# Kernel tuning notes

Measured on AMD Instinct MI355X. Metric: run time of the kernel, lower is better.

## Reference

```python
import jax, jax.numpy as jnp
import numpy as np

NUM_MEL = 80
STACK_FRAMES = 4   # encoder.embed.right_context + 1
STRIDE = 4         # encoder.embed.subsampling_rate
N_SUB = 1          # n_subsequent
NCB = 1            # num_codebooks
EMB_DIM = 16
NUM_EMB = 8192
ENC_DIM = 512
B, T = 16, 2048
T_ENC = (T - STACK_FRAMES) // STRIDE + 1  # 512
EPS_LN = 1e-6


def setup_inputs() -> dict:
    key = jax.random.key(0)
    k = jax.random.split(key, 6)
    feats = jax.random.normal(k[0], (B, T, NUM_MEL), dtype=jnp.float32)
    feats_lengths = jax.random.randint(k[1], (B,), T // 2, T + 1, dtype=jnp.int32)
    encoder_out = jax.random.normal(k[2], (B, T_ENC, ENC_DIM), dtype=jnp.float32)
    in_dim = NUM_MEL * STRIDE
    lim = float(np.sqrt(6.0 / (in_dim + EMB_DIM * NCB)))  # xavier-uniform
    projection = jax.random.uniform(k[3], (in_dim, EMB_DIM * NCB), jnp.float32, -lim, lim)
    emb = jax.random.normal(k[4], (NUM_EMB, NCB, EMB_DIM), dtype=jnp.float32)
    embeddings = emb / (jnp.linalg.norm(emb, axis=-1, keepdims=True) + 1e-8)
    top_n_out = 0.02 * jax.random.normal(k[5], (N_SUB, NCB, ENC_DIM, NUM_EMB), dtype=jnp.float32)
    return {"feats": feats, "feats_lengths": feats_lengths, "encoder_out": encoder_out,
            "projection": projection, "embeddings": embeddings, "top_n_out": top_n_out}


def _stack_features(feats, lens):
    b, t, f = feats.shape
    n = (t - STACK_FRAMES) // STRIDE + 1
    idx = jnp.arange(n)[:, None] * STRIDE + jnp.arange(STACK_FRAMES)[None, :]  # [n, S]
    stack = feats[:, idx, :].reshape(b, n, STACK_FRAMES * f)                   # [B, n, S*F]
    mask = jnp.arange(t)[None, :] < lens[:, None]                              # [B, T]
    sub_mask = jnp.all(mask[:, idx], axis=-1)                                  # [B, n]
    mean = stack.mean(-1, keepdims=True)
    var = stack.var(-1, keepdims=True)
    stack = (stack - mean) * jax.lax.rsqrt(var + EPS_LN)  # LayerNorm, no affine
    return stack, sub_mask


def _nearest_idx(stack, projection, embeddings):
    x = stack @ projection                                         # [B, n, ncb*E]
    x = x / (jnp.linalg.norm(x, axis=-1, keepdims=True) + 1e-8)
    b, n, _ = x.shape
    v, ncb, e = embeddings.shape
    xf = x.reshape(b * n, ncb, e)
    dots = jnp.einsum('nce,vce->ncv', xf, embeddings)              # [N, ncb, V]
    x2 = jnp.sum(xf * xf, -1, keepdims=True)                       # [N, ncb, 1]
    e2 = jnp.sum(embeddings * embeddings, -1).T[None]              # [1, ncb, V]
    dist = x2 - 2.0 * dots + e2
    codes = jnp.argmin(dist, axis=-1)                              # [N, ncb]
    return codes.reshape(b, n, ncb)


def _forward(feats, feats_lengths, encoder_out, projection, embeddings, top_n_out):
    stack, stack_mask = _stack_features(feats, feats_lengths)
    target = _nearest_idx(stack, projection, embeddings)           # [B, n, ncb]
    tq = stack_mask.shape[1]
    # unfold(n_subsequent=1) -> [B, Tq, ns, ncb]
    target = target[:, :tq, None, :]
    # encoder output mask (subsampled lengths)
    t_enc = encoder_out.shape[1]
    out_mask = jnp.arange(t_enc)[None, :] < (feats_lengths // STRIDE)[:, None]
    logits = jnp.einsum('btd,scdv->bsctv', encoder_out, top_n_out)  # [B, ns, ncb, T', V]
    logits = logits[:, :, :, :tq, :][:, :, :, :-1, :]               # frames 0..Tq-2
    target = target[:, 1:]                                          # targets 1..Tq-1
    masks = (out_mask[:, :tq] & stack_mask)[:, 1:]                  # [B, Tq-1] bool
    mf = masks.astype(logits.dtype)
    logp = jax.nn.log_softmax(logits, axis=-1)
    tgt_bsct = jnp.transpose(target, (0, 2, 3, 1))                  # [B, ns, ncb, Tq-1]
    nll = -jnp.take_along_axis(logp, tgt_bsct[..., None], axis=-1)[..., 0]
    mfull = jnp.broadcast_to(mf[:, None, None, :], nll.shape)
    loss = (nll * mfull).sum() / mfull.sum()
    num_codes = mf.sum() * NCB
    pred = jnp.argmax(logits, axis=-1)                              # [B, ns, ncb, Tq-1]
    corr = (pred == tgt_bsct).astype(logits.dtype)
    codes_acc = (corr * mfull).sum() / num_codes
    masked_tgt = target * masks[:, :, None, None].astype(target.dtype)
    presence = jnp.zeros((NUM_EMB,), jnp.int32).at[masked_tgt.reshape(-1)].set(1)
    uniq_num_codes = presence.sum().astype(jnp.float32)
    return loss, codes_acc, num_codes, uniq_num_codes


def reference(feats, feats_lengths, encoder_out, projection, embeddings, top_n_out):
    return _forward(feats, feats_lengths, encoder_out, projection, embeddings, top_n_out)
```

## Files before the change

### kernel.cpp

```cpp
#include <hip/hip_runtime.h>
#include <math.h>

typedef __attribute__((ext_vector_type(4))) float f32x4;
typedef __attribute__((ext_vector_type(8))) short bf16x8;

#define NB 16
#define NT 2048
#define NMEL 80
#define NPOS 512
#define EDIM 16
#define NEMB 8192
#define ENCD 512
#define MROWS (NB*511)
#define MPAD 8192
#define NVT 64

__device__ __forceinline__ unsigned short f2bf(float x) {
    union { float f; unsigned u; } v; v.f = x;
    unsigned r = v.u + 0x7fffu + ((v.u >> 16) & 1u);
    return (unsigned short)(r >> 16);
}

__device__ __forceinline__ void gl_lds16(const void* gsrc, void* lds) {
    __builtin_amdgcn_global_load_lds(
        (const __attribute__((address_space(1))) unsigned int*)gsrc,
        (__attribute__((address_space(3))) unsigned int*)lds,
        16, 0, 0);
}

__global__ __launch_bounds__(256) void prep_kernel(
    const float* __restrict__ feats, const float* __restrict__ proj,
    const float* __restrict__ emb, const float* __restrict__ enc,
    const float* __restrict__ tno,
    unsigned short* __restrict__ ynB, unsigned short* __restrict__ embB,
    float* __restrict__ h2, int* __restrict__ presence,
    unsigned char* __restrict__ encF8, unsigned char* __restrict__ tnoF8)
{
    __shared__ float tileT[32][33];
    const int bid = blockIdx.x;
    const int tid = threadIdx.x;

    if (bid < 512) {
        const int lane = tid & 63;
        const int wave = tid >> 6;
        const int gbase = bid * 16 + wave * 4;
        if (bid < 32) presence[bid * 256 + tid] = 0;

        float yn[4][EDIM];
        #pragma unroll
        for (int pi = 0; pi < 4; ++pi) {
            const int g = gbase + pi;
            const int b = g >> 9;
            const int i = g & 511;
            float xv[5];
            float s = 0.f, sq = 0.f;
            #pragma unroll
            for (int qq = 0; qq < 5; ++qq) {
                const int d = lane + 64 * qq;
                const int j = d / 80, k = d - j * 80;
                const float v = feats[((b * NT) + (i * 4 + j)) * NMEL + k];
                xv[qq] = v; s += v; sq += v * v;
            }
            for (int m = 1; m < 64; m <<= 1) { s += __shfl_xor(s, m); sq += __shfl_xor(sq, m); }
            const float mean = s * (1.0f / 320.0f);
            const float var  = sq * (1.0f / 320.0f) - mean * mean;
            const float rstd = rsqrtf(var + 1e-6f);
            float acc[EDIM];
            #pragma unroll
            for (int e = 0; e < EDIM; ++e) acc[e] = 0.f;
            #pragma unroll
            for (int qq = 0; qq < 5; ++qq) {
                const int d = lane + 64 * qq;
                const float xn = (xv[qq] - mean) * rstd;
                #pragma unroll
                for (int e = 0; e < EDIM; ++e) acc[e] += xn * proj[d * EDIM + e];
            }
            for (int m = 1; m < 64; m <<= 1) {
                #pragma unroll
                for (int e = 0; e < EDIM; ++e) acc[e] += __shfl_xor(acc[e], m);
            }
            float nsq = 0.f;
            #pragma unroll
            for (int e = 0; e < EDIM; ++e) nsq += acc[e] * acc[e];
            const float inv = 1.0f / (sqrtf(nsq) + 1e-8f);
            #pragma unroll
            for (int e = 0; e < EDIM; ++e) yn[pi][e] = acc[e] * inv;
        }
        #pragma unroll
        for (int pi = 0; pi < 4; ++pi) {
            if (lane == pi) {
                unsigned short* dst = &ynB[(size_t)(gbase + pi) * 32];
                #pragma unroll
                for (int e = 0; e < EDIM; ++e) dst[e] = f2bf(yn[pi][e]);
                #pragma unroll
                for (int e = EDIM; e < 32; ++e) dst[e] = 0;
            }
        }
    } else if (bid < 1024) {
        const int bid2 = bid - 512;
        const int lane = tid & 63;
        #pragma unroll
        for (int pass = 0; pass < 4; ++pass) {
            const int m = bid2 * 16 + pass * 4 + (tid >> 6);
            const int d = lane * 8;
            uint2 o = make_uint2(0u, 0u);
            if (m < MROWS) {
                const int b = m / 511, t = m - b * 511;
                const float4 f0 = *(const float4*)&enc[((size_t)(b * 512 + t)) * ENCD + d];
                const float4 f1 = *(const float4*)&enc[((size_t)(b * 512 + t)) * ENCD + d + 4];
                int w0 = __builtin_amdgcn_cvt_pk_fp8_f32(f0.x, f0.y, 0, false);
                w0     = __builtin_amdgcn_cvt_pk_fp8_f32(f0.z, f0.w, w0, true);
                int w1 = __builtin_amdgcn_cvt_pk_fp8_f32(f1.x, f1.y, 0, false);
                w1     = __builtin_amdgcn_cvt_pk_fp8_f32(f1.z, f1.w, w1, true);
                o.x = (unsigned)w0; o.y = (unsigned)w1;
            }
            *(uint2*)&encF8[(size_t)m * ENCD + d] = o;
        }
    } else if (bid < 2048) {
        const int bid2 = bid - 1024;
        const int tx = tid & 31, ty = tid >> 5;
        const int np = tid >> 3, kc = tid & 7;
        #pragma unroll
        for (int it = 0; it < 4; ++it) {
            const int tile = bid2 * 4 + it;
            const int n0 = (tile & 255) * 32;
            const int k0 = (tile >> 8) * 32;
            __syncthreads();
            #pragma unroll
            for (int i = 0; i < 4; ++i)
                tileT[ty + 8 * i][tx] = tno[(size_t)(k0 + ty + 8 * i) * NEMB + n0 + tx];
            __syncthreads();
            const float t0 = 16.0f * tileT[kc * 4 + 0][np];
            const float t1 = 16.0f * tileT[kc * 4 + 1][np];
            const float t2 = 16.0f * tileT[kc * 4 + 2][np];
            const float t3 = 16.0f * tileT[kc * 4 + 3][np];
            int w = __builtin_amdgcn_cvt_pk_fp8_f32(t0, t1, 0, false);
            w     = __builtin_amdgcn_cvt_pk_fp8_f32(t2, t3, w, true);
            ((unsigned*)tnoF8)[(size_t)(n0 + np) * (ENCD / 4) + (k0 >> 2) + kc] = (unsigned)w;
        }
    } else {
        const int row = (bid - 2048) * 256 + tid;
        const float* ep = &emb[(size_t)row * EDIM];
        const float4 e0 = *(const float4*)&ep[0];
        const float4 e1 = *(const float4*)&ep[4];
        const float4 e2v = *(const float4*)&ep[8];
        const float4 e3 = *(const float4*)&ep[12];
        const float e2 = e0.x*e0.x + e0.y*e0.y + e0.z*e0.z + e0.w*e0.w
                       + e1.x*e1.x + e1.y*e1.y + e1.z*e1.z + e1.w*e1.w
                       + e2v.x*e2v.x + e2v.y*e2v.y + e2v.z*e2v.z + e2v.w*e2v.w
                       + e3.x*e3.x + e3.y*e3.y + e3.z*e3.z + e3.w*e3.w;
        h2[row] = 0.5f * e2;
        unsigned short* dst = &embB[(size_t)row * 32];
        dst[0]  = f2bf(e0.x); dst[1]  = f2bf(e0.y); dst[2]  = f2bf(e0.z); dst[3]  = f2bf(e0.w);
        dst[4]  = f2bf(e1.x); dst[5]  = f2bf(e1.y); dst[6]  = f2bf(e1.z); dst[7]  = f2bf(e1.w);
        dst[8]  = f2bf(e2v.x); dst[9]  = f2bf(e2v.y); dst[10] = f2bf(e2v.z); dst[11] = f2bf(e2v.w);
        dst[12] = f2bf(e3.x); dst[13] = f2bf(e3.y); dst[14] = f2bf(e3.z); dst[15] = f2bf(e3.w);
        #pragma unroll
        for (int e = EDIM; e < 32; ++e) dst[e] = 0;
    }
}

__global__ __launch_bounds__(256) void codes_mfma(
    const unsigned short* __restrict__ ynB, const unsigned short* __restrict__ embB,
    const float* __restrict__ h2,
    float* __restrict__ pscore, int* __restrict__ pcidx)
{
    const int tid = threadIdx.x;
    const int lane = tid & 63;
    const int wave = tid >> 6;
    const int pgrp  = blockIdx.x >> 2;
    const int chunk = blockIdx.x & 3;
    const int p0 = pgrp * 64 + wave * 16;
    const int l15 = lane & 15, q = lane >> 4;

    const bf16x8 a = *(const bf16x8*)&ynB[(size_t)(p0 + l15) * 32 + q * 8];

    float mn[4]; int mi[4];
    #pragma unroll
    for (int r = 0; r < 4; ++r) { mn[r] = INFINITY; mi[r] = 0x7fffffff; }

    const int e0 = chunk * 2048;
    #pragma unroll 4
    for (int g = 0; g < 128; ++g) {
        const int eidx = e0 + g * 16 + l15;
        const bf16x8 b = *(const bf16x8*)&embB[(size_t)eidx * 32 + q * 8];
        const float hv = h2[eidx];
        f32x4 d = __builtin_amdgcn_mfma_f32_16x16x32_bf16(a, b, (f32x4){0.f, 0.f, 0.f, 0.f}, 0, 0, 0);
        #pragma unroll
        for (int r = 0; r < 4; ++r) {
            const float sc = hv - d[r];
            if (sc < mn[r]) { mn[r] = sc; mi[r] = eidx; }
        }
    }
    #pragma unroll
    for (int m = 1; m < 16; m <<= 1) {
        #pragma unroll
        for (int r = 0; r < 4; ++r) {
            const float ov = __shfl_xor(mn[r], m);
            const int   oi = __shfl_xor(mi[r], m);
            if (ov < mn[r] || (ov == mn[r] && oi < mi[r])) { mn[r] = ov; mi[r] = oi; }
        }
    }
    if (l15 == 0) {
        #pragma unroll
        for (int r = 0; r < 4; ++r) {
            pscore[chunk * MPAD + p0 + q * 4 + r] = mn[r];
            pcidx [chunk * MPAD + p0 + q * 4 + r] = mi[r];
        }
    }
}

__global__ __launch_bounds__(256) void codes_merge(
    const float* __restrict__ pscore, const int* __restrict__ pcidx,
    int* __restrict__ codes)
{
    const int g = blockIdx.x * 256 + threadIdx.x;
    float m = INFINITY; int mi = 0x7fffffff;
    #pragma unroll
    for (int c = 0; c < 4; ++c) {
        const float s = pscore[c * MPAD + g];
        const int  ix = pcidx [c * MPAD + g];
        if (s < m || (s == m && ix < mi)) { m = s; mi = ix; }
    }
    codes[g] = mi;
}

__global__ __launch_bounds__(256, 3) void logits_mfma(
    const unsigned char* __restrict__ encF8, const unsigned char* __restrict__ tnoF8,
    const int* __restrict__ codes,
    float* __restrict__ pm, float* __restrict__ ps, int* __restrict__ pidx,
    float* __restrict__ tgtlog)
{
    __shared__ __align__(16) unsigned char As3[3][128 * 64];
    __shared__ __align__(16) unsigned char Bs3[3][128 * 64];
    __shared__ float redM[2][128];
    __shared__ float redS[2][128];
    __shared__ int   redI[2][128];

    const int tid  = threadIdx.x;
    const int lane = tid & 63;
    const int wave = tid >> 6;
    const int wr = wave >> 1, wc = wave & 1;

    const int bid = blockIdx.x;
    const int xcd = bid & 7;
    const int idx = bid >> 3;
    const int mt  = xcd * 8 + (idx & 7);
    const int vt  = idx >> 3;
    const int m0 = mt * 128, n0 = vt * 128;

    const int rb   = lane >> 2;
    const int gcB  = ((lane & 3) ^ ((lane >> 3) & 3)) * 16;
    const size_t abase0 = (size_t)(m0 + wave * 32 + rb) * ENCD + gcB;
    const size_t bbase0 = (size_t)(n0 + wave * 32 + rb) * ENCD + gcB;

#define STAGE(t, buf)                                                                        \
    {                                                                                        \
        const int k0s = (t) * 64;                                                            \
        gl_lds16(encF8 + abase0 + k0s,              &As3[buf][(wave * 32) * 64]);            \
        gl_lds16(tnoF8 + bbase0 + k0s,              &Bs3[buf][(wave * 32) * 64]);            \
        gl_lds16(encF8 + abase0 + 16 * ENCD + k0s,  &As3[buf][(wave * 32 + 16) * 64]);       \
        gl_lds16(tnoF8 + bbase0 + 16 * ENCD + k0s,  &Bs3[buf][(wave * 32 + 16) * 64]);       \
    }

    f32x4 acc[4][4];
    #pragma unroll
    for (int i = 0; i < 4; ++i)
        #pragma unroll
        for (int j = 0; j < 4; ++j)
            acc[i][j] = (f32x4){0.f, 0.f, 0.f, 0.f};

    const int l15 = lane & 15, q = lane >> 4;
    const int rsw = (l15 >> 1) & 3;

    STAGE(0, 0);
    STAGE(1, 1);

    #pragma unroll
    for (int t = 0; t < 8; ++t) {
        if (t < 7) { asm volatile("s_waitcnt vmcnt(4)" ::: "memory"); }
        else       { asm volatile("s_waitcnt vmcnt(0)" ::: "memory"); }
        __builtin_amdgcn_s_barrier();
        __builtin_amdgcn_sched_barrier(0);
        if (t + 2 < 8) {
            const int nb = (t + 2) % 3;
            STAGE(t + 2, nb);
        }
        const unsigned char* Ab = As3[t % 3];
        const unsigned char* Bb = Bs3[t % 3];
        #pragma unroll
        for (int ks = 0; ks < 2; ++ks) {
            const int co = ((ks * 2 + (q >> 1)) ^ rsw) * 16 + (q & 1) * 8;
            long a[4], b[4];
            #pragma unroll
            for (int mi = 0; mi < 4; ++mi)
                a[mi] = *(const long*)&Ab[(wr * 64 + mi * 16 + l15) * 64 + co];
            #pragma unroll
            for (int ni = 0; ni < 4; ++ni)
                b[ni] = *(const long*)&Bb[(wc * 64 + ni * 16 + l15) * 64 + co];
            __builtin_amdgcn_s_setprio(1);
            #pragma unroll
            for (int mi = 0; mi < 4; ++mi)
                #pragma unroll
                for (int ni = 0; ni < 4; ++ni)
                    acc[mi][ni] = __builtin_amdgcn_mfma_f32_16x16x32_fp8_fp8(a[mi], b[ni], acc[mi][ni], 0, 0, 0);
            __builtin_amdgcn_s_setprio(0);
        }
    }
#undef STAGE

    #pragma unroll
    for (int mi = 0; mi < 4; ++mi)
        #pragma unroll
        for (int ni = 0; ni < 4; ++ni)
            acc[mi][ni] *= 0.0625f;

    #pragma unroll
    for (int mi = 0; mi < 4; ++mi) {
        #pragma unroll
        for (int r = 0; r < 4; ++r) {
            const int rl = wr * 64 + mi * 16 + q * 4 + r;
            float lm = -INFINITY; int li = 0;
            #pragma unroll
            for (int ni = 0; ni < 4; ++ni) {
                const float v = acc[mi][ni][r];
                const int col = wc * 64 + ni * 16 + l15;
                if (v > lm) { lm = v; li = col; }
            }
            #pragma unroll
            for (int mk = 8; mk >= 1; mk >>= 1) {
                const float ov = __shfl_xor(lm, mk);
                const int   oi = __shfl_xor(li, mk);
                if (ov > lm || (ov == lm && oi < li)) { lm = ov; li = oi; }
            }
            float le = 0.f;
            #pragma unroll
            for (int ni = 0; ni < 4; ++ni) le += __expf(acc[mi][ni][r] - lm);
            #pragma unroll
            for (int mk = 8; mk >= 1; mk >>= 1) le += __shfl_xor(le, mk);

            if (l15 == 0) { redM[wc][rl] = lm; redS[wc][rl] = le; redI[wc][rl] = li; }

            const int mg = m0 + rl;
            if (mg < MROWS) {
                const int bb = mg / 511, tt = mg - bb * 511;
                const int tv = codes[bb * NPOS + tt + 1];
                const int rel = tv - n0 - wc * 64;
                #pragma unroll
                for (int ni = 0; ni < 4; ++ni) {
                    if (rel >= ni * 16 && rel < ni * 16 + 16 && (rel & 15) == l15)
                        tgtlog[mg] = acc[mi][ni][r];
                }
            }
        }
    }
    __syncthreads();
    if (tid < 128) {
        const int rl = tid;
        const int mg = m0 + rl;
        if (mg < MROWS) {
            const float mA = redM[0][rl], mB = redM[1][rl];
            const int   iA = redI[0][rl], iB = redI[1][rl];
            float gm; int gi;
            if (mB > mA || (mB == mA && iB + 64 < iA)) { gm = mB; gi = 64 + iB; } else { gm = mA; gi = iA; }
            const float S = redS[0][rl] * __expf(mA - gm) + redS[1][rl] * __expf(mB - gm);
            pm[(size_t)vt * MPAD + mg]   = gm;
            ps[(size_t)vt * MPAD + mg]   = S;
            pidx[(size_t)vt * MPAD + mg] = n0 + gi;
        }
    }
}

__global__ __launch_bounds__(256) void combine_kernel(
    const float* __restrict__ pm, const float* __restrict__ ps,
    const int* __restrict__ pidx, const float* __restrict__ tgtlog,
    const int* __restrict__ codes, const int* __restrict__ lens,
    float* __restrict__ rnll, float* __restrict__ rcorr, float* __restrict__ rmf,
    int* __restrict__ presence)
{
    const int g = blockIdx.x * 256 + threadIdx.x;
    if (g >= MROWS) return;
    float gm = -INFINITY; int gi = 0;
    #pragma unroll 8
    for (int nt = 0; nt < NVT; ++nt) {
        const float v = pm[(size_t)nt * MPAD + g];
        if (v > gm) { gm = v; gi = pidx[(size_t)nt * MPAD + g]; }
    }
    float S = 0.f;
    #pragma unroll 8
    for (int nt = 0; nt < NVT; ++nt) S += ps[(size_t)nt * MPAD + g] * __expf(pm[(size_t)nt * MPAD + g] - gm);
    const float lse = gm + logf(S);
    const int b = g / 511, t = g - b * 511;
    const int tv = codes[b * NPOS + t + 1];
    const float nll = lse - tgtlog[g];
    const int L = lens[b];
    const int s = t + 1;
    const bool mf = (s < (L / 4)) && (4 * s + 3 < L);
    rnll[g]  = mf ? nll : 0.f;
    rcorr[g] = (mf && gi == tv) ? 1.f : 0.f;
    rmf[g]   = mf ? 1.f : 0.f;
    if (mf) presence[tv] = 1;
}

__global__ __launch_bounds__(256) void finalize_kernel(
    const float* __restrict__ rnll, const float* __restrict__ rcorr,
    const float* __restrict__ rmf, const int* __restrict__ presence,
    float* __restrict__ out)
{
    __shared__ float sh0[256], sh1[256], sh2[256];
    __shared__ int shp[256];
    const int tid = threadIdx.x;
    float sn = 0.f, sc = 0.f, sm = 0.f; int pp = 0;
    for (int g = tid; g < MROWS; g += 256) { sn += rnll[g]; sc += rcorr[g]; sm += rmf[g]; }
    for (int v = tid; v < NEMB; v += 256) pp += presence[v];
    sh0[tid] = sn; sh1[tid] = sc; sh2[tid] = sm; shp[tid] = pp;
    __syncthreads();
    for (int s = 128; s > 0; s >>= 1) {
        if (tid < s) { sh0[tid] += sh0[tid + s]; sh1[tid] += sh1[tid + s]; sh2[tid] += sh2[tid + s]; shp[tid] += shp[tid + s]; }
        __syncthreads();
    }
    if (tid == 0) {
        const float Sm = sh2[0];
        out[0] = sh0[0] / Sm;
        out[1] = sh1[0] / Sm;
        out[2] = Sm;
        out[3] = (float)shp[0];
    }
}

extern "C" void kernel_launch(void* const* d_in, const int* in_sizes, int n_in,
                              void* d_out, int out_size, void* d_ws, size_t ws_size,
                              hipStream_t stream) {
    const float* feats = (const float*)d_in[0];
    const int*   lens  = (const int*)d_in[1];
    const float* enc   = (const float*)d_in[2];
    const float* proj  = (const float*)d_in[3];
    const float* emb   = (const float*)d_in[4];
    const float* tno   = (const float*)d_in[5];
    float* out = (float*)d_out;

    int* codes          = (int*)d_ws;
    int* presence       = codes + MPAD;
    float* pm           = (float*)(presence + MPAD);
    float* ps           = pm + (size_t)NVT * MPAD;
    int* pidx           = (int*)(ps + (size_t)NVT * MPAD);
    float* tgtlog       = (float*)(pidx + (size_t)NVT * MPAD);
    float* rnll         = tgtlog + MPAD;
    float* rcorr        = rnll + MPAD;
    float* rmf          = rcorr + MPAD;
    float* pscore       = rmf + MPAD;
    int*   pcidx        = (int*)(pscore + 4 * MPAD);
    float* h2           = (float*)(pcidx + 4 * MPAD);
    unsigned short* ynB  = (unsigned short*)(h2 + MPAD);
    unsigned short* embB = ynB + (size_t)MPAD * 32;
    unsigned char* encF8 = (unsigned char*)(embB + (size_t)MPAD * 32);
    unsigned char* tnoF8 = encF8 + (size_t)MPAD * ENCD;

    hipLaunchKernelGGL(prep_kernel, dim3(2080), dim3(256), 0, stream,
                       feats, proj, emb, enc, tno, ynB, embB, h2, presence, encF8, tnoF8);
    hipLaunchKernelGGL(codes_mfma, dim3(512), dim3(256), 0, stream, ynB, embB, h2, pscore, pcidx);
    hipLaunchKernelGGL(codes_merge, dim3(32), dim3(256), 0, stream, pscore, pcidx, codes);
    hipLaunchKernelGGL(logits_mfma, dim3(64 * 64), dim3(256), 0, stream, encF8, tnoF8, codes, pm, ps, pidx, tgtlog);
    hipLaunchKernelGGL(combine_kernel, dim3((MROWS + 255) / 256), dim3(256), 0, stream,
                       pm, ps, pidx, tgtlog, codes, lens, rnll, rcorr, rmf, presence);
    hipLaunchKernelGGL(finalize_kernel, dim3(1), dim3(256), 0, stream, rnll, rcorr, rmf, presence, out);
}
```

Measured before the change: 224.0 us.

## Load A operand directly into registers with prefetch, drop A LDS staging

```diff
diff --git a/kernel.cpp b/kernel.cpp
--- a/kernel.cpp
+++ b/kernel.cpp
@@ -225,13 +225,12 @@
     codes[g] = mi;
 }
 
-__global__ __launch_bounds__(256, 3) void logits_mfma(
+__global__ __launch_bounds__(256, 4) void logits_mfma(
     const unsigned char* __restrict__ encF8, const unsigned char* __restrict__ tnoF8,
     const int* __restrict__ codes,
     float* __restrict__ pm, float* __restrict__ ps, int* __restrict__ pidx,
     float* __restrict__ tgtlog)
 {
-    __shared__ __align__(16) unsigned char As3[3][128 * 64];
     __shared__ __align__(16) unsigned char Bs3[3][128 * 64];
     __shared__ float redM[2][128];
     __shared__ float redS[2][128];
@@ -251,15 +250,12 @@
 
     const int rb   = lane >> 2;
     const int gcB  = ((lane & 3) ^ ((lane >> 3) & 3)) * 16;
-    const size_t abase0 = (size_t)(m0 + wave * 32 + rb) * ENCD + gcB;
     const size_t bbase0 = (size_t)(n0 + wave * 32 + rb) * ENCD + gcB;
 
 #define STAGE(t, buf)                                                                        \
     {                                                                                        \
         const int k0s = (t) * 64;                                                            \
-        gl_lds16(encF8 + abase0 + k0s,              &As3[buf][(wave * 32) * 64]);            \
         gl_lds16(tnoF8 + bbase0 + k0s,              &Bs3[buf][(wave * 32) * 64]);            \
-        gl_lds16(encF8 + abase0 + 16 * ENCD + k0s,  &As3[buf][(wave * 32 + 16) * 64]);       \
         gl_lds16(tnoF8 + bbase0 + 16 * ENCD + k0s,  &Bs3[buf][(wave * 32 + 16) * 64]);       \
     }
 
@@ -273,28 +269,40 @@
     const int l15 = lane & 15, q = lane >> 4;
     const int rsw = (l15 >> 1) & 3;
 
+    const unsigned char* arow[4];
+    #pragma unroll
+    for (int mi = 0; mi < 4; ++mi)
+        arow[mi] = encF8 + (size_t)(m0 + wr * 64 + mi * 16 + l15) * ENCD + q * 8;
+
+    long aC[4][2], aN[4][2];
+
     STAGE(0, 0);
     STAGE(1, 1);
+    #pragma unroll
+    for (int mi = 0; mi < 4; ++mi) {
+        aC[mi][0] = *(const long*)(arow[mi] + 0);
+        aC[mi][1] = *(const long*)(arow[mi] + 32);
+    }
 
     #pragma unroll
     for (int t = 0; t < 8; ++t) {
-        if (t < 7) { asm volatile("s_waitcnt vmcnt(4)" ::: "memory"); }
+        if (t < 7) { asm volatile("s_waitcnt vmcnt(10)" ::: "memory"); }
         else       { asm volatile("s_waitcnt vmcnt(0)" ::: "memory"); }
         __builtin_amdgcn_s_barrier();
         __builtin_amdgcn_sched_barrier(0);
-        if (t + 2 < 8) {
-            const int nb = (t + 2) % 3;
-            STAGE(t + 2, nb);
-        }
-        const unsigned char* Ab = As3[t % 3];
+        if (t + 2 < 8) STAGE(t + 2, (t + 2) % 3);
+        if (t + 1 < 8) {
+            #pragma unroll
+            for (int mi = 0; mi < 4; ++mi) {
+                aN[mi][0] = *(const long*)(arow[mi] + (t + 1) * 64);
+                aN[mi][1] = *(const long*)(arow[mi] + (t + 1) * 64 + 32);
+            }
+        }
         const unsigned char* Bb = Bs3[t % 3];
         #pragma unroll
         for (int ks = 0; ks < 2; ++ks) {
             const int co = ((ks * 2 + (q >> 1)) ^ rsw) * 16 + (q & 1) * 8;
-            long a[4], b[4];
-            #pragma unroll
-            for (int mi = 0; mi < 4; ++mi)
-                a[mi] = *(const long*)&Ab[(wr * 64 + mi * 16 + l15) * 64 + co];
+            long b[4];
             #pragma unroll
             for (int ni = 0; ni < 4; ++ni)
                 b[ni] = *(const long*)&Bb[(wc * 64 + ni * 16 + l15) * 64 + co];
@@ -303,8 +311,12 @@
             for (int mi = 0; mi < 4; ++mi)
                 #pragma unroll
                 for (int ni = 0; ni < 4; ++ni)
-                    acc[mi][ni] = __builtin_amdgcn_mfma_f32_16x16x32_fp8_fp8(a[mi], b[ni], acc[mi][ni], 0, 0, 0);
+                    acc[mi][ni] = __builtin_amdgcn_mfma_f32_16x16x32_fp8_fp8(aC[mi][ks], b[ni], acc[mi][ni], 0, 0, 0);
             __builtin_amdgcn_s_setprio(0);
+        }
+        if (t + 1 < 8) {
+            #pragma unroll
+            for (int mi = 0; mi < 4; ++mi) { aC[mi][0] = aN[mi][0]; aC[mi][1] = aN[mi][1]; }
         }
     }
 #undef STAGE
```

After: 265.9 us. +18.7%, slower.
